# Kernel tuning notes

Hardware: AMD Instinct MI355X
Metric: run time of the kernel (lower is better)

Reference implementation:

```python
import jax, jax.numpy as jnp
import numpy as np

B, I, H, O = 64, 2048, 2048, 2048


def setup_inputs() -> dict:
    key = jax.random.key(0)
    ks = jax.random.split(key, 17)
    s = 0.02  # keep activations in a sane range
    return {
        "x": jax.random.normal(ks[0], (B, I), jnp.float32),
        "h_prev": jax.random.normal(ks[1], (B, H), jnp.float32),
        "c_prev": jax.random.normal(ks[2], (B, H), jnp.float32),
        "Wfh": jax.random.normal(ks[3], (H, H), jnp.float32) * s,
        "Wfx": jax.random.normal(ks[4], (I, H), jnp.float32) * s,
        "bf": jax.random.normal(ks[5], (H,), jnp.float32) * s,
        "Wih": jax.random.normal(ks[6], (H, H), jnp.float32) * s,
        "Wix": jax.random.normal(ks[7], (I, H), jnp.float32) * s,
        "bi": jax.random.normal(ks[8], (H,), jnp.float32) * s,
        "Woh": jax.random.normal(ks[9], (H, H), jnp.float32) * s,
        "Wox": jax.random.normal(ks[10], (I, H), jnp.float32) * s,
        "bo": jax.random.normal(ks[11], (H,), jnp.float32) * s,
        "Wch": jax.random.normal(ks[12], (H, H), jnp.float32) * s,
        "Wcx": jax.random.normal(ks[13], (I, H), jnp.float32) * s,
        "bc": jax.random.normal(ks[14], (H,), jnp.float32) * s,
        "Wy": jax.random.normal(ks[15], (H, O), jnp.float32) * s,
        "by": jax.random.normal(ks[16], (O,), jnp.float32) * s,
    }


def reference(x, h_prev, c_prev, Wfh, Wfx, bf, Wih, Wix, bi,
              Woh, Wox, bo, Wch, Wcx, bc, Wy, by):
    # Fused single-step LSTM cell: concat the 4 per-gate matmuls into
    # two GEMMs ([B,H]@[H,4H] and [B,I]@[I,4H]) -- same math as the
    # original 8 separate matmuls, gate order (f, i, c~, o).
    Wh = jnp.concatenate([Wfh, Wih, Wch, Woh], axis=1)  # [H, 4H]
    Wx = jnp.concatenate([Wfx, Wix, Wcx, Wox], axis=1)  # [I, 4H]
    b = jnp.concatenate([bf, bi, bc, bo], axis=0)       # [4H]
    gates = h_prev @ Wh + x @ Wx + b                     # [B, 4H]
    f_, i_, ct_, o_ = jnp.split(gates, 4, axis=1)
    f = jax.nn.sigmoid(f_)
    i = jax.nn.sigmoid(i_)
    ct = jnp.tanh(ct_)
    o = jax.nn.sigmoid(o_)
    c = f * c_prev + i * ct
    h = o * jnp.tanh(c)
    # NOTE: original computes y from the PREVIOUS hidden state (hList[-1])
    y = h_prev @ Wy + by
    # Pack (y, h_new, c_new) along feature dim (O == H) for a single output.
    return jnp.concatenate([y, h, c], axis=-1)  # [B, O + 2H]
```

## Files before the change

### kernel.cpp

```cpp
#include <hip/hip_runtime.h>

typedef short  bf16x8  __attribute__((ext_vector_type(8)));
typedef float  f32x4   __attribute__((ext_vector_type(4)));
typedef float  f32x16  __attribute__((ext_vector_type(16)));
typedef unsigned short ushort;

__device__ __forceinline__ short f2bf(float f) {
  __bf16 h = (__bf16)f;
  return __builtin_bit_cast(short, h);
}

#define GATE_PART 0
#define Y_PART    4194304
#define ABF_OFF   5242880

__global__ __launch_bounds__(256) void lstm_aconv(
    const float* __restrict__ X, const float* __restrict__ H,
    ushort* __restrict__ Abf)
{
  const int t  = blockIdx.x * 256 + threadIdx.x;
  const int e0 = t * 8;
  const int b  = e0 >> 12;
  const int k  = e0 & 4095;
  const float* src = (k < 2048) ? (H + (size_t)b * 2048 + k)
                                : (X + (size_t)b * 2048 + (k - 2048));
  f32x4 v0 = *(const f32x4*)(src);
  f32x4 v1 = *(const f32x4*)(src + 4);
  bf16x8 o;
  o[0] = f2bf(v0[0]); o[1] = f2bf(v0[1]); o[2] = f2bf(v0[2]); o[3] = f2bf(v0[3]);
  o[4] = f2bf(v1[0]); o[5] = f2bf(v1[1]); o[6] = f2bf(v1[2]); o[7] = f2bf(v1[3]);
  *(bf16x8*)(Abf + e0) = o;
}

template<int NSTEPS>
__device__ __forceinline__ void gemm_wave(
    const float* __restrict__ wbase,
    const ushort* __restrict__ a0p, const ushort* __restrict__ a1p,
    float bias, float* __restrict__ outBase, int outStride, int lane)
{
  constexpr int D = 4;
  const int kg8 = (lane >> 5) << 3;
  const float* wcol = wbase + (size_t)kg8 * 2048;

  f32x16 acc0, acc1;
  #pragma unroll
  for (int r = 0; r < 16; ++r) { acc0[r] = bias; acc1[r] = bias; }

  float wf[D][8]; bf16x8 a0r[D], a1r[D];

  #pragma unroll
  for (int d = 0; d < D; ++d) {
    const float* p = wcol + (size_t)(d * 16) * 2048;
    #pragma unroll
    for (int i = 0; i < 8; ++i) wf[d][i] = p[(size_t)i * 2048];
    a0r[d] = *(const bf16x8*)(a0p + d * 16);
    a1r[d] = *(const bf16x8*)(a1p + d * 16);
  }

  #pragma unroll
  for (int s = 0; s < NSTEPS; ++s) {
    const int slot = s & (D - 1);
    bf16x8 bf;
    #pragma unroll
    for (int i = 0; i < 8; ++i) bf[i] = f2bf(wf[slot][i]);
    acc0 = __builtin_amdgcn_mfma_f32_32x32x16_bf16(a0r[slot], bf, acc0, 0, 0, 0);
    acc1 = __builtin_amdgcn_mfma_f32_32x32x16_bf16(a1r[slot], bf, acc1, 0, 0, 0);
    if (s + D < NSTEPS) {
      const float* p = wcol + (size_t)((s + D) * 16) * 2048;
      #pragma unroll
      for (int i = 0; i < 8; ++i) wf[slot][i] = p[(size_t)i * 2048];
      a0r[slot] = *(const bf16x8*)(a0p + (s + D) * 16);
      a1r[slot] = *(const bf16x8*)(a1p + (s + D) * 16);
    }
  }

  const int rbase = 4 * (lane >> 5);
  #pragma unroll
  for (int r = 0; r < 16; ++r) {
    const int row = (r & 3) + 8 * (r >> 2) + rbase;
    outBase[(size_t)row * outStride]        = acc0[r];
    outBase[(size_t)(row + 32) * outStride] = acc1[r];
  }
}

__global__ __launch_bounds__(256, 3) void lstm_gemm(
    const float* __restrict__ Wfh, const float* __restrict__ Wfx, const float* __restrict__ bfp,
    const float* __restrict__ Wih, const float* __restrict__ Wix, const float* __restrict__ bip,
    const float* __restrict__ Woh, const float* __restrict__ Wox, const float* __restrict__ bop,
    const float* __restrict__ Wch, const float* __restrict__ Wcx, const float* __restrict__ bcp,
    const float* __restrict__ Wy,  const float* __restrict__ by,
    float* __restrict__ ws)
{
  const int lane = threadIdx.x & 63;
  const int w    = blockIdx.x * 4 + (threadIdx.x >> 6);
  const int n    = lane & 31;
  const int kg8  = (lane >> 5) << 3;
  const ushort* Abf = (const ushort*)(ws + ABF_OFF);

  if (w < 2048) {
    const int gate = w >> 9;
    const int ks   = (w >> 6) & 7;
    const int jt   = w & 63;
    const int j0   = jt * 32;

    const float *Wg_h, *Wg_x, *bg;
    if      (gate == 0) { Wg_h = Wfh; Wg_x = Wfx; bg = bfp; }
    else if (gate == 1) { Wg_h = Wih; Wg_x = Wix; bg = bip; }
    else if (gate == 2) { Wg_h = Wch; Wg_x = Wcx; bg = bcp; }
    else                { Wg_h = Woh; Wg_x = Wox; bg = bop; }

    const float* Wmat = (ks < 4) ? Wg_h : Wg_x;
    const int krow0 = (ks & 3) * 512;
    const int aK0   = ks * 512;
    const float bias = (ks == 0) ? bg[j0 + n] : 0.f;

    const float* wbase = Wmat + (size_t)krow0 * 2048 + j0 + n;
    const ushort* a0p = Abf + (size_t)(lane & 31) * 4096 + aK0 + kg8;
    const ushort* a1p = a0p + (size_t)32 * 4096;
    float* outBase = ws + GATE_PART + (size_t)ks * 524288 + gate * 2048 + j0 + n;

    gemm_wave<32>(wbase, a0p, a1p, bias, outBase, 8192, lane);
  } else {
    const int yi  = w - 2048;
    const int ksy = yi >> 6;
    const int jt  = yi & 63;
    const int j0  = jt * 32;

    const int krow0 = ksy * 256;
    const float bias = (ksy == 0) ? by[j0 + n] : 0.f;

    const float* wbase = Wy + (size_t)krow0 * 2048 + j0 + n;
    const ushort* a0p = Abf + (size_t)(lane & 31) * 4096 + krow0 + kg8;
    const ushort* a1p = a0p + (size_t)32 * 4096;
    float* outBase = ws + Y_PART + (size_t)ksy * 131072 + j0 + n;

    gemm_wave<16>(wbase, a0p, a1p, bias, outBase, 2048, lane);
  }
}

__device__ __forceinline__ float fsigmoid(float x) {
  return 1.f / (1.f + __expf(-x));
}
__device__ __forceinline__ float ftanh(float x) {
  return 1.f - 2.f / (1.f + __expf(2.f * x));
}

__global__ __launch_bounds__(64) void lstm_combine(
    const float* __restrict__ ws, const float* __restrict__ c_prev,
    float* __restrict__ out)
{
  const int t  = blockIdx.x * 64 + threadIdx.x;
  const int b  = t >> 9;
  const int j4 = (t & 511) * 4;

  f32x4 g[4];
  #pragma unroll
  for (int gg = 0; gg < 4; ++gg) {
    f32x4 s = (f32x4){0.f, 0.f, 0.f, 0.f};
    #pragma unroll
    for (int ks = 0; ks < 8; ++ks)
      s += *(const f32x4*)(ws + GATE_PART + (size_t)ks * 524288 + (size_t)b * 8192 + gg * 2048 + j4);
    g[gg] = s;
  }
  f32x4 ysum = (f32x4){0.f, 0.f, 0.f, 0.f};
  #pragma unroll
  for (int ks = 0; ks < 8; ++ks)
    ysum += *(const f32x4*)(ws + Y_PART + (size_t)ks * 131072 + (size_t)b * 2048 + j4);

  const f32x4 cp = *(const f32x4*)(c_prev + (size_t)b * 2048 + j4);
  f32x4 hF, cF;
  #pragma unroll
  for (int e = 0; e < 4; ++e) {
    float f  = fsigmoid(g[0][e]);
    float i  = fsigmoid(g[1][e]);
    float ct = ftanh(g[2][e]);
    float o  = fsigmoid(g[3][e]);
    float c  = f * cp[e] + i * ct;
    cF[e] = c;
    hF[e] = o * ftanh(c);
  }
  float* ob = out + (size_t)b * 6144;
  *(f32x4*)(ob + j4)        = ysum;
  *(f32x4*)(ob + 2048 + j4) = hF;
  *(f32x4*)(ob + 4096 + j4) = cF;
}

extern "C" void kernel_launch(void* const* d_in, const int* in_sizes, int n_in,
                              void* d_out, int out_size, void* d_ws, size_t ws_size,
                              hipStream_t stream)
{
  const float* X   = (const float*)d_in[0];
  const float* H   = (const float*)d_in[1];
  const float* Cp  = (const float*)d_in[2];
  const float* Wfh = (const float*)d_in[3];
  const float* Wfx = (const float*)d_in[4];
  const float* bfp = (const float*)d_in[5];
  const float* Wih = (const float*)d_in[6];
  const float* Wix = (const float*)d_in[7];
  const float* bip = (const float*)d_in[8];
  const float* Woh = (const float*)d_in[9];
  const float* Wox = (const float*)d_in[10];
  const float* bop = (const float*)d_in[11];
  const float* Wch = (const float*)d_in[12];
  const float* Wcx = (const float*)d_in[13];
  const float* bcp = (const float*)d_in[14];
  const float* Wy  = (const float*)d_in[15];
  const float* by  = (const float*)d_in[16];
  float* ws  = (float*)d_ws;
  float* out = (float*)d_out;

  lstm_aconv<<<128, 256, 0, stream>>>(X, H, (ushort*)(ws + ABF_OFF));
  lstm_gemm<<<640, 256, 0, stream>>>(Wfh, Wfx, bfp, Wih, Wix, bip,
                                     Woh, Wox, bop, Wch, Wcx, bcp, Wy, by, ws);
  lstm_combine<<<512, 64, 0, stream>>>(ws, Cp, out);
}
```

Baseline: 216.2 us.

## Stage weight and activation tiles through LDS with async global_load_lds double buffering

Each GEMM block now handles a 128-column stripe and one K-split instead of one wave per 32-column tile. Its four waves cooperatively copy 64-row weight chunks and swizzled bf16 activation chunks into LDS using global_load_lds, double-buffered with explicit vmcnt waits and barriers. The goal is to replace strided per-lane scalar global weight loads with coalesced 16-byte transfers that overlap with MFMA work. The costs are about 80KB of LDS per block, lower occupancy (launch bounds 2), and hand-written waitcnt counts that must match the number of issued loads. The grid size is unchanged at 640 blocks and now maps to 512 gate blocks plus 128 y blocks.

```diff
diff --git a/kernel.cpp b/kernel.cpp
--- a/kernel.cpp
+++ b/kernel.cpp
@@ -1,4 +1,7 @@
 #include <hip/hip_runtime.h>
+
+#define GAS __attribute__((address_space(1)))
+#define LAS __attribute__((address_space(3)))
 
 typedef short  bf16x8  __attribute__((ext_vector_type(8)));
 typedef float  f32x4   __attribute__((ext_vector_type(4)));
@@ -32,58 +35,7 @@
   *(bf16x8*)(Abf + e0) = o;
 }
 
-template<int NSTEPS>
-__device__ __forceinline__ void gemm_wave(
-    const float* __restrict__ wbase,
-    const ushort* __restrict__ a0p, const ushort* __restrict__ a1p,
-    float bias, float* __restrict__ outBase, int outStride, int lane)
-{
-  constexpr int D = 4;
-  const int kg8 = (lane >> 5) << 3;
-  const float* wcol = wbase + (size_t)kg8 * 2048;
-
-  f32x16 acc0, acc1;
-  #pragma unroll
-  for (int r = 0; r < 16; ++r) { acc0[r] = bias; acc1[r] = bias; }
-
-  float wf[D][8]; bf16x8 a0r[D], a1r[D];
-
-  #pragma unroll
-  for (int d = 0; d < D; ++d) {
-    const float* p = wcol + (size_t)(d * 16) * 2048;
-    #pragma unroll
-    for (int i = 0; i < 8; ++i) wf[d][i] = p[(size_t)i * 2048];
-    a0r[d] = *(const bf16x8*)(a0p + d * 16);
-    a1r[d] = *(const bf16x8*)(a1p + d * 16);
-  }
-
-  #pragma unroll
-  for (int s = 0; s < NSTEPS; ++s) {
-    const int slot = s & (D - 1);
-    bf16x8 bf;
-    #pragma unroll
-    for (int i = 0; i < 8; ++i) bf[i] = f2bf(wf[slot][i]);
-    acc0 = __builtin_amdgcn_mfma_f32_32x32x16_bf16(a0r[slot], bf, acc0, 0, 0, 0);
-    acc1 = __builtin_amdgcn_mfma_f32_32x32x16_bf16(a1r[slot], bf, acc1, 0, 0, 0);
-    if (s + D < NSTEPS) {
-      const float* p = wcol + (size_t)((s + D) * 16) * 2048;
-      #pragma unroll
-      for (int i = 0; i < 8; ++i) wf[slot][i] = p[(size_t)i * 2048];
-      a0r[slot] = *(const bf16x8*)(a0p + (s + D) * 16);
-      a1r[slot] = *(const bf16x8*)(a1p + (s + D) * 16);
-    }
-  }
-
-  const int rbase = 4 * (lane >> 5);
-  #pragma unroll
-  for (int r = 0; r < 16; ++r) {
-    const int row = (r & 3) + 8 * (r >> 2) + rbase;
-    outBase[(size_t)row * outStride]        = acc0[r];
-    outBase[(size_t)(row + 32) * outStride] = acc1[r];
-  }
-}
-
-__global__ __launch_bounds__(256, 3) void lstm_gemm(
+__global__ __launch_bounds__(256, 2) void lstm_gemm(
     const float* __restrict__ Wfh, const float* __restrict__ Wfx, const float* __restrict__ bfp,
     const float* __restrict__ Wih, const float* __restrict__ Wix, const float* __restrict__ bip,
     const float* __restrict__ Woh, const float* __restrict__ Wox, const float* __restrict__ bop,
@@ -91,50 +43,118 @@
     const float* __restrict__ Wy,  const float* __restrict__ by,
     float* __restrict__ ws)
 {
-  const int lane = threadIdx.x & 63;
-  const int w    = blockIdx.x * 4 + (threadIdx.x >> 6);
+  __shared__ float  ldsW[2][64 * 128];
+  __shared__ ushort ldsA[2][64 * 64];
+
+  const int tid  = threadIdx.x;
+  const int lane = tid & 63;
+  const int widx = tid >> 6;
   const int n    = lane & 31;
   const int kg8  = (lane >> 5) << 3;
+  const int j0w  = widx * 32;
   const ushort* Abf = (const ushort*)(ws + ABF_OFF);
 
-  if (w < 2048) {
-    const int gate = w >> 9;
-    const int ks   = (w >> 6) & 7;
-    const int jt   = w & 63;
-    const int j0   = jt * 32;
-
+  const int bid = blockIdx.x;
+  const float* Wmat; int krow0m, aK0, nch;
+  float bias; float* outBase; int outStride;
+
+  if (bid < 512) {
+    const int gate   = bid >> 7;
+    const int stripe = (bid >> 3) & 15;
+    const int ks     = bid & 7;
+    const int j0     = stripe * 128;
     const float *Wg_h, *Wg_x, *bg;
     if      (gate == 0) { Wg_h = Wfh; Wg_x = Wfx; bg = bfp; }
     else if (gate == 1) { Wg_h = Wih; Wg_x = Wix; bg = bip; }
     else if (gate == 2) { Wg_h = Wch; Wg_x = Wcx; bg = bcp; }
     else                { Wg_h = Woh; Wg_x = Wox; bg = bop; }
-
-    const float* Wmat = (ks < 4) ? Wg_h : Wg_x;
-    const int krow0 = (ks & 3) * 512;
-    const int aK0   = ks * 512;
-    const float bias = (ks == 0) ? bg[j0 + n] : 0.f;
-
-    const float* wbase = Wmat + (size_t)krow0 * 2048 + j0 + n;
-    const ushort* a0p = Abf + (size_t)(lane & 31) * 4096 + aK0 + kg8;
-    const ushort* a1p = a0p + (size_t)32 * 4096;
-    float* outBase = ws + GATE_PART + (size_t)ks * 524288 + gate * 2048 + j0 + n;
-
-    gemm_wave<32>(wbase, a0p, a1p, bias, outBase, 8192, lane);
+    Wmat    = ((ks < 4) ? Wg_h : Wg_x) + j0;
+    krow0m  = (ks & 3) * 512;
+    aK0     = ks * 512;
+    nch     = 8;
+    bias    = (ks == 0) ? bg[j0 + j0w + n] : 0.f;
+    outBase = ws + GATE_PART + (size_t)ks * 524288 + (size_t)gate * 2048 + j0 + j0w + n;
+    outStride = 8192;
   } else {
-    const int yi  = w - 2048;
-    const int ksy = yi >> 6;
-    const int jt  = yi & 63;
-    const int j0  = jt * 32;
-
-    const int krow0 = ksy * 256;
-    const float bias = (ksy == 0) ? by[j0 + n] : 0.f;
-
-    const float* wbase = Wy + (size_t)krow0 * 2048 + j0 + n;
-    const ushort* a0p = Abf + (size_t)(lane & 31) * 4096 + krow0 + kg8;
-    const ushort* a1p = a0p + (size_t)32 * 4096;
-    float* outBase = ws + Y_PART + (size_t)ksy * 131072 + j0 + n;
-
-    gemm_wave<16>(wbase, a0p, a1p, bias, outBase, 2048, lane);
+    const int yi     = bid - 512;
+    const int stripe = yi >> 3;
+    const int ksy    = yi & 7;
+    const int j0     = stripe * 128;
+    Wmat    = Wy + j0;
+    krow0m  = ksy * 256;
+    aK0     = krow0m;
+    nch     = 4;
+    bias    = (ksy == 0) ? by[j0 + j0w + n] : 0.f;
+    outBase = ws + Y_PART + (size_t)ksy * 131072 + j0 + j0w + n;
+    outStride = 2048;
+  }
+
+  auto stageW = [&](int buf, int krow) {
+    #pragma unroll
+    for (int i = 0; i < 8; ++i) {
+      const int r = i * 8 + widx * 2 + (lane >> 5);
+      const float* src = Wmat + (size_t)(krow + r) * 2048 + (lane & 31) * 4;
+      float* dst = &ldsW[buf][(i * 8 + widx * 2) * 128];
+      __builtin_amdgcn_global_load_lds((const GAS unsigned*)src,
+                                       (LAS unsigned*)dst, 16, 0, 0);
+    }
+  };
+  auto stageA = [&](int buf, int aK) {
+    #pragma unroll
+    for (int i = 0; i < 2; ++i) {
+      const int b    = i * 32 + widx * 8 + (lane >> 3);
+      const int coff = (((lane & 7) * 16) ^ ((b & 7) << 4)) >> 1;
+      const ushort* src = Abf + (size_t)b * 4096 + aK + coff;
+      ushort* dst = &ldsA[buf][(i * 32 + widx * 8) * 64];
+      __builtin_amdgcn_global_load_lds((const GAS unsigned*)src,
+                                       (LAS unsigned*)dst, 16, 0, 0);
+    }
+  };
+
+  f32x16 acc0, acc1;
+  #pragma unroll
+  for (int r = 0; r < 16; ++r) { acc0[r] = bias; acc1[r] = bias; }
+
+  stageW(0, krow0m); stageA(0, aK0);
+
+  for (int ch = 0; ch < nch; ++ch) {
+    if (ch + 1 < nch) {
+      stageW((ch + 1) & 1, krow0m + (ch + 1) * 64);
+      stageA((ch + 1) & 1, aK0 + (ch + 1) * 64);
+      asm volatile("s_waitcnt vmcnt(10)" ::: "memory");
+    } else {
+      asm volatile("s_waitcnt vmcnt(0)" ::: "memory");
+    }
+    __builtin_amdgcn_s_barrier();
+
+    {
+      const int buf = ch & 1;
+      const char* ab = (const char*)&ldsA[buf][0];
+      #pragma unroll
+      for (int k0 = 0; k0 < 64; k0 += 16) {
+        const int kk = k0 + kg8;
+        float wf[8];
+        #pragma unroll
+        for (int i = 0; i < 8; ++i)
+          wf[i] = ldsW[buf][(kk + i) * 128 + j0w + n];
+        bf16x8 bfrag;
+        #pragma unroll
+        for (int i = 0; i < 8; ++i) bfrag[i] = f2bf(wf[i]);
+        bf16x8 a0 = *(const bf16x8*)(ab + (((n)      * 128 + kk * 2) ^ ((n & 7) << 4)));
+        bf16x8 a1 = *(const bf16x8*)(ab + (((n + 32) * 128 + kk * 2) ^ ((n & 7) << 4)));
+        acc0 = __builtin_amdgcn_mfma_f32_32x32x16_bf16(a0, bfrag, acc0, 0, 0, 0);
+        acc1 = __builtin_amdgcn_mfma_f32_32x32x16_bf16(a1, bfrag, acc1, 0, 0, 0);
+      }
+    }
+    __builtin_amdgcn_s_barrier();
+  }
+
+  const int rbase = 4 * (lane >> 5);
+  #pragma unroll
+  for (int r = 0; r < 16; ++r) {
+    const int row = (r & 3) + 8 * (r >> 2) + rbase;
+    outBase[(size_t)row * outStride]        = acc0[r];
+    outBase[(size_t)(row + 32) * outStride] = acc1[r];
   }
 }
 
```

Result: faster. 203.2 us (-6.0%).
